# Kernel tuning notes

Hardware: AMD Instinct MI355X
Metric: run time of the kernel (lower is better)

## Reference

```python
import jax, jax.numpy as jnp
import numpy as np


def setup_inputs() -> dict:
    key = jax.random.key(0)
    k1, k2 = jax.random.split(key)
    B, T, D, K = 16, 800, 256, 64
    x = jax.random.normal(k1, (B, T, D), dtype=jnp.float32)
    mu = jax.random.normal(k2, (K, D), dtype=jnp.float32)
    prec = jnp.ones((K,), dtype=jnp.float32)
    return {"x": x, "mu": mu, "prec": prec}


def reference(x, mu, prec):
    # x: (B,T,D), mu: (K,D), prec: (K,)
    delta = x[:, :, None, :] - mu[None, None, :, :]          # (B,T,K,D)
    dist = jnp.sum(delta * delta, axis=-1)                   # (B,T,K) dist_pow=2
    llk = -(prec * prec) * dist                              # use_bias=False -> bias=0
    r = jax.nn.softmax(llk, axis=-1)                         # softmax over components K
    r = r / (jnp.sum(r, axis=1, keepdims=True) + 1e-9)       # normalize over time T
    pool = jnp.einsum('btk,btkd->bkd', r, delta)             # weighted sum over T
    return pool.reshape(x.shape[0], -1)                      # (B, K*D)
```

## Files before the change

### kernel.cpp

```cpp
#include <hip/hip_runtime.h>

#define B_ 16
#define T_ 800
#define D_ 256
#define K_ 64
#define NTILE 13

typedef __attribute__((ext_vector_type(8))) short short8v;
typedef __attribute__((ext_vector_type(4))) float f32x4v;

__device__ __forceinline__ ushort bf16rn(float v) {
    unsigned int b = __float_as_uint(v);
    return (ushort)((b + 0x7fffu + ((b >> 16) & 1u)) >> 16);
}
__device__ __forceinline__ float bf16hi(ushort h) {
    return __uint_as_float(((unsigned int)h) << 16);
}

__global__ __launch_bounds__(256) void prep(
    const float* __restrict__ x, const float* __restrict__ mu, const float* __restrict__ prec,
    float* __restrict__ xx_g, float* __restrict__ mm_g, float* __restrict__ p2_g)
{
    const int bid = blockIdx.x, tid = threadIdx.x;
    if (bid < 3200) {
        const int row = bid * 4 + (tid >> 6), lane = tid & 63;
        float4 v = ((const float4*)x)[(size_t)row * 64 + lane];
        float s = v.x*v.x + v.y*v.y + v.z*v.z + v.w*v.w;
        #pragma unroll
        for (int off = 32; off > 0; off >>= 1) s += __shfl_xor(s, off);
        if (lane == 0) xx_g[row] = s;
    } else if (bid < 3216) {
        const int row = (bid - 3200) * 4 + (tid >> 6), lane = tid & 63;
        float4 v = ((const float4*)mu)[(size_t)row * 64 + lane];
        float s = v.x*v.x + v.y*v.y + v.z*v.z + v.w*v.w;
        #pragma unroll
        for (int off = 32; off > 0; off >>= 1) s += __shfl_xor(s, off);
        if (lane == 0) mm_g[row] = s;
    } else {
        if (tid < 64) { float p = prec[tid]; p2_g[tid] = p * p; }
    }
}

__global__ __launch_bounds__(256, 1) void kernelAB(
    const float* __restrict__ x, const float* __restrict__ mu,
    const float* __restrict__ xx_g, const float* __restrict__ mm_g,
    const float* __restrict__ p2_g,
    float* __restrict__ Pp, float* __restrict__ Spart)
{
    __shared__ ushort xh_s[64 * 264];
    __shared__ ushort xl_s[64 * 264];
    __shared__ ushort muh_s[64 * 264];
    __shared__ ushort mul_s[64 * 264];
    __shared__ ushort rtT_s[64 * 72];
    __shared__ float xxs[64], mms[64], p2s[64];
    __shared__ float sred[4][64];

    const int tid  = threadIdx.x;
    const int lane = tid & 63;
    const int w    = tid >> 6;
    const int m    = lane & 15;
    const int q    = lane >> 4;
    const int b    = blockIdx.x / NTILE;
    const int tile = blockIdx.x % NTILE;
    const int t0   = tile * 64;

    if (tid < 64)       xxs[tid]       = xx_g[b * T_ + min(t0 + tid, T_ - 1)];
    else if (tid < 128) mms[tid - 64]  = mm_g[tid - 64];
    else if (tid < 192) p2s[tid - 128] = p2_g[tid - 128];

    #pragma unroll 4
    for (int jj = 0; jj < 16; ++jj) {
        const int idx = tid + jj * 256;
        const int row = idx >> 6, c = idx & 63;
        int trow = t0 + row; if (trow > T_ - 1) trow = T_ - 1;
        float4 v = ((const float4*)x)[(size_t)(b * T_ + trow) * 64 + c];
        ushort4 h, l;
        h.x = bf16rn(v.x); l.x = bf16rn(v.x - bf16hi(h.x));
        h.y = bf16rn(v.y); l.y = bf16rn(v.y - bf16hi(h.y));
        h.z = bf16rn(v.z); l.z = bf16rn(v.z - bf16hi(h.z));
        h.w = bf16rn(v.w); l.w = bf16rn(v.w - bf16hi(h.w));
        *(ushort4*)&xh_s[row * 264 + c * 4] = h;
        *(ushort4*)&xl_s[row * 264 + c * 4] = l;
    }
    #pragma unroll 4
    for (int jj = 0; jj < 16; ++jj) {
        const int idx = tid + jj * 256;
        const int row = idx >> 6, c = idx & 63;
        float4 v = ((const float4*)mu)[(size_t)row * 64 + c];
        ushort4 h, l;
        h.x = bf16rn(v.x); l.x = bf16rn(v.x - bf16hi(h.x));
        h.y = bf16rn(v.y); l.y = bf16rn(v.y - bf16hi(h.y));
        h.z = bf16rn(v.z); l.z = bf16rn(v.z - bf16hi(h.z));
        h.w = bf16rn(v.w); l.w = bf16rn(v.w - bf16hi(h.w));
        *(ushort4*)&muh_s[row * 264 + c * 4] = h;
        *(ushort4*)&mul_s[row * 264 + c * 4] = l;
    }
    __syncthreads();

    f32x4v acc[4];
    #pragma unroll
    for (int nt = 0; nt < 4; ++nt) acc[nt] = (f32x4v){0.f, 0.f, 0.f, 0.f};

    #pragma unroll 2
    for (int c = 0; c < 8; ++c) {
        const int ao = (w * 16 + m) * 264 + c * 32 + q * 8;
        short8v ah = *(const short8v*)&xh_s[ao];
        short8v al = *(const short8v*)&xl_s[ao];
        #pragma unroll
        for (int nt = 0; nt < 4; ++nt) {
            const int bo = (nt * 16 + m) * 264 + c * 32 + q * 8;
            short8v bh = *(const short8v*)&muh_s[bo];
            short8v bl = *(const short8v*)&mul_s[bo];
            acc[nt] = __builtin_amdgcn_mfma_f32_16x16x32_bf16(ah, bh, acc[nt], 0, 0, 0);
            acc[nt] = __builtin_amdgcn_mfma_f32_16x16x32_bf16(ah, bl, acc[nt], 0, 0, 0);
            acc[nt] = __builtin_amdgcn_mfma_f32_16x16x32_bf16(al, bh, acc[nt], 0, 0, 0);
        }
    }

    float mmk[4], p2k[4];
    #pragma unroll
    for (int nt = 0; nt < 4; ++nt) { mmk[nt] = mms[nt * 16 + m]; p2k[nt] = p2s[nt * 16 + m]; }

    ushort4 rp[4];
    float sacc[4] = {0.f, 0.f, 0.f, 0.f};
    #pragma unroll
    for (int r = 0; r < 4; ++r) {
        const int tl = w * 16 + q * 4 + r;
        const float xxv = xxs[tl];
        const bool valid = (t0 + tl) < T_;
        float llk[4];
        #pragma unroll
        for (int nt = 0; nt < 4; ++nt)
            llk[nt] = p2k[nt] * (2.f * acc[nt][r] - xxv - mmk[nt]);
        float mx = fmaxf(fmaxf(llk[0], llk[1]), fmaxf(llk[2], llk[3]));
        mx = fmaxf(mx, __shfl_xor(mx, 1)); mx = fmaxf(mx, __shfl_xor(mx, 2));
        mx = fmaxf(mx, __shfl_xor(mx, 4)); mx = fmaxf(mx, __shfl_xor(mx, 8));
        float e[4], ps = 0.f;
        #pragma unroll
        for (int nt = 0; nt < 4; ++nt) { e[nt] = __expf(llk[nt] - mx); ps += e[nt]; }
        ps += __shfl_xor(ps, 1); ps += __shfl_xor(ps, 2);
        ps += __shfl_xor(ps, 4); ps += __shfl_xor(ps, 8);
        const float inv = valid ? (1.f / ps) : 0.f;
        #pragma unroll
        for (int nt = 0; nt < 4; ++nt) {
            float rv = e[nt] * inv;
            sacc[nt] += rv;
            ((ushort*)&rp[nt])[r] = bf16rn(rv);
        }
    }
    #pragma unroll
    for (int nt = 0; nt < 4; ++nt)
        *(ushort4*)&rtT_s[(nt * 16 + m) * 72 + w * 16 + q * 4] = rp[nt];
    #pragma unroll
    for (int nt = 0; nt < 4; ++nt) {
        sacc[nt] += __shfl_xor(sacc[nt], 16);
        sacc[nt] += __shfl_xor(sacc[nt], 32);
    }
    if (q == 0) {
        #pragma unroll
        for (int nt = 0; nt < 4; ++nt) sred[w][nt * 16 + m] = sacc[nt];
    }
    __syncthreads();

    if (tid < 64) {
        float s = sred[0][tid] + sred[1][tid] + sred[2][tid] + sred[3][tid];
        Spart[((size_t)b * NTILE + tile) * K_ + tid] = s;
    }

    {
        const int tp = tid & 31, dg = tid >> 5;
        #pragma unroll
        for (int c = 0; c < 4; ++c) {
            short8v a0 = *(const short8v*)&xh_s[(2 * tp)     * 264 + dg * 32 + c * 8];
            short8v a1 = *(const short8v*)&xh_s[(2 * tp + 1) * 264 + dg * 32 + c * 8];
            short8v b0 = *(const short8v*)&xl_s[(2 * tp)     * 264 + dg * 32 + c * 8];
            short8v b1 = *(const short8v*)&xl_s[(2 * tp + 1) * 264 + dg * 32 + c * 8];
            #pragma unroll
            for (int j = 0; j < 8; ++j) {
                const int d = dg * 32 + c * 8 + j;
                const int widx = (tp & 3) + 4 * ((tp >> 2) ^ (d & 7));
                ushort2 hv, lv;
                hv.x = (ushort)a0[j]; hv.y = (ushort)a1[j];
                lv.x = (ushort)b0[j]; lv.y = (ushort)b1[j];
                *(ushort2*)&muh_s[d * 64 + widx * 2] = hv;
                *(ushort2*)&mul_s[d * 64 + widx * 2] = lv;
            }
        }
    }
    __syncthreads();

    f32x4v acc2[16];
    #pragma unroll
    for (int nt = 0; nt < 16; ++nt) acc2[nt] = (f32x4v){0.f, 0.f, 0.f, 0.f};

    #pragma unroll
    for (int tc = 0; tc < 2; ++tc) {
        short8v ar = *(const short8v*)&rtT_s[(w * 16 + m) * 72 + tc * 32 + q * 8];
        #pragma unroll
        for (int nt = 0; nt < 16; ++nt) {
            const int drow = nt * 16 + m;
            const int eoff = ((tc * 4 + q) ^ (drow & 7)) * 8;
            short8v bh = *(const short8v*)&muh_s[drow * 64 + eoff];
            short8v bl = *(const short8v*)&mul_s[drow * 64 + eoff];
            acc2[nt] = __builtin_amdgcn_mfma_f32_16x16x32_bf16(ar, bh, acc2[nt], 0, 0, 0);
            acc2[nt] = __builtin_amdgcn_mfma_f32_16x16x32_bf16(ar, bl, acc2[nt], 0, 0, 0);
        }
    }

    float* Pb = Pp + ((size_t)(b * NTILE + tile)) * K_ * D_;
    #pragma unroll
    for (int nt = 0; nt < 16; ++nt) {
        #pragma unroll
        for (int r = 0; r < 4; ++r)
            Pb[(size_t)(w * 16 + q * 4 + r) * D_ + nt * 16 + m] = acc2[nt][r];
    }
}

__global__ __launch_bounds__(256) void kernelC(
    const float* __restrict__ Pp, const float* __restrict__ Spart,
    const float* __restrict__ mu, float* __restrict__ out)
{
    const int o4 = blockIdx.x * 256 + threadIdx.x;
    const int d4 = o4 & 63;
    const int k  = (o4 >> 6) & 63;
    const int b  = o4 >> 12;

    float s = 0.f;
    #pragma unroll
    for (int p = 0; p < NTILE; ++p)
        s += Spart[((size_t)b * NTILE + p) * K_ + k];

    float4 acc = make_float4(0.f, 0.f, 0.f, 0.f);
    #pragma unroll
    for (int p = 0; p < NTILE; ++p) {
        float4 v = ((const float4*)Pp)[((size_t)(b * NTILE + p) * K_ + k) * (D_ / 4) + d4];
        acc.x += v.x; acc.y += v.y; acc.z += v.z; acc.w += v.w;
    }
    const float inv = 1.f / (s + 1e-9f);
    const float sm  = s * inv;
    const float4 m = ((const float4*)mu)[k * 64 + d4];
    float4 o;
    o.x = acc.x * inv - sm * m.x;
    o.y = acc.y * inv - sm * m.y;
    o.z = acc.z * inv - sm * m.z;
    o.w = acc.w * inv - sm * m.w;
    ((float4*)out)[o4] = o;
}

extern "C" void kernel_launch(void* const* d_in, const int* in_sizes, int n_in,
                              void* d_out, int out_size, void* d_ws, size_t ws_size,
                              hipStream_t stream) {
    const float* x    = (const float*)d_in[0];
    const float* mu   = (const float*)d_in[1];
    const float* prec = (const float*)d_in[2];
    float* out = (float*)d_out;

    float* Pp    = (float*)d_ws;
    float* Spart = Pp + (size_t)B_ * NTILE * K_ * D_;
    float* xx_g  = Spart + (size_t)B_ * NTILE * K_;
    float* mm_g  = xx_g + (size_t)B_ * T_;
    float* p2_g  = mm_g + 64;

    prep<<<3217, 256, 0, stream>>>(x, mu, prec, xx_g, mm_g, p2_g);
    kernelAB<<<B_ * NTILE, 256, 0, stream>>>(x, mu, xx_g, mm_g, p2_g, Pp, Spart);
    kernelC<<<256, 256, 0, stream>>>(Pp, Spart, mu, out);
}
```

Before: 80.27 us.

## Fuse norm prep into main kernel and double block to 512 threads

Removes the separate prep kernel by computing row squared norms of x and mu during the shared-memory staging loads, and computes prec squared in-kernel. The main kernel now runs 512 threads per block: each of the 8 waves handles half the components in the distance GEMM and half the D columns in the pooling GEMM. The softmax max and sum are combined across the two wave halves through shared memory with extra barriers. This saves a kernel launch and a pass over x and aims for more latency hiding per block, at the cost of added synchronisation.

Result: no change. 80.42 us (+0.2%).

```diff
diff --git a/kernel.cpp b/kernel.cpp
--- a/kernel.cpp
+++ b/kernel.cpp
@@ -17,34 +17,9 @@
     return __uint_as_float(((unsigned int)h) << 16);
 }
 
-__global__ __launch_bounds__(256) void prep(
-    const float* __restrict__ x, const float* __restrict__ mu, const float* __restrict__ prec,
-    float* __restrict__ xx_g, float* __restrict__ mm_g, float* __restrict__ p2_g)
-{
-    const int bid = blockIdx.x, tid = threadIdx.x;
-    if (bid < 3200) {
-        const int row = bid * 4 + (tid >> 6), lane = tid & 63;
-        float4 v = ((const float4*)x)[(size_t)row * 64 + lane];
-        float s = v.x*v.x + v.y*v.y + v.z*v.z + v.w*v.w;
-        #pragma unroll
-        for (int off = 32; off > 0; off >>= 1) s += __shfl_xor(s, off);
-        if (lane == 0) xx_g[row] = s;
-    } else if (bid < 3216) {
-        const int row = (bid - 3200) * 4 + (tid >> 6), lane = tid & 63;
-        float4 v = ((const float4*)mu)[(size_t)row * 64 + lane];
-        float s = v.x*v.x + v.y*v.y + v.z*v.z + v.w*v.w;
-        #pragma unroll
-        for (int off = 32; off > 0; off >>= 1) s += __shfl_xor(s, off);
-        if (lane == 0) mm_g[row] = s;
-    } else {
-        if (tid < 64) { float p = prec[tid]; p2_g[tid] = p * p; }
-    }
-}
-
-__global__ __launch_bounds__(256, 1) void kernelAB(
+__global__ __launch_bounds__(512, 1) void kernelAB(
     const float* __restrict__ x, const float* __restrict__ mu,
-    const float* __restrict__ xx_g, const float* __restrict__ mm_g,
-    const float* __restrict__ p2_g,
+    const float* __restrict__ prec,
     float* __restrict__ Pp, float* __restrict__ Spart)
 {
     __shared__ ushort xh_s[64 * 264];
@@ -53,6 +28,7 @@
     __shared__ ushort mul_s[64 * 264];
     __shared__ ushort rtT_s[64 * 72];
     __shared__ float xxs[64], mms[64], p2s[64];
+    __shared__ float red_m[64][2], red_s[64][2];
     __shared__ float sred[4][64];
 
     const int tid  = threadIdx.x;
@@ -64,101 +40,132 @@
     const int tile = blockIdx.x % NTILE;
     const int t0   = tile * 64;
 
-    if (tid < 64)       xxs[tid]       = xx_g[b * T_ + min(t0 + tid, T_ - 1)];
-    else if (tid < 128) mms[tid - 64]  = mm_g[tid - 64];
-    else if (tid < 192) p2s[tid - 128] = p2_g[tid - 128];
+    if (tid < 64) { float p = prec[tid]; p2s[tid] = p * p; }
 
     #pragma unroll 4
-    for (int jj = 0; jj < 16; ++jj) {
-        const int idx = tid + jj * 256;
-        const int row = idx >> 6, c = idx & 63;
+    for (int jj = 0; jj < 8; ++jj) {
+        const int idx = tid + jj * 512;
+        const int row = idx >> 6;
+        const int cc  = idx & 63;
         int trow = t0 + row; if (trow > T_ - 1) trow = T_ - 1;
-        float4 v = ((const float4*)x)[(size_t)(b * T_ + trow) * 64 + c];
+        float4 v = ((const float4*)x)[(size_t)(b * T_ + trow) * 64 + cc];
+        float sq = v.x*v.x + v.y*v.y + v.z*v.z + v.w*v.w;
+        #pragma unroll
+        for (int off = 32; off > 0; off >>= 1) sq += __shfl_xor(sq, off);
+        if (lane == 0) xxs[row] = sq;
         ushort4 h, l;
         h.x = bf16rn(v.x); l.x = bf16rn(v.x - bf16hi(h.x));
         h.y = bf16rn(v.y); l.y = bf16rn(v.y - bf16hi(h.y));
         h.z = bf16rn(v.z); l.z = bf16rn(v.z - bf16hi(h.z));
         h.w = bf16rn(v.w); l.w = bf16rn(v.w - bf16hi(h.w));
-        *(ushort4*)&xh_s[row * 264 + c * 4] = h;
-        *(ushort4*)&xl_s[row * 264 + c * 4] = l;
+        *(ushort4*)&xh_s[row * 264 + cc * 4] = h;
+        *(ushort4*)&xl_s[row * 264 + cc * 4] = l;
     }
     #pragma unroll 4
-    for (int jj = 0; jj < 16; ++jj) {
-        const int idx = tid + jj * 256;
-        const int row = idx >> 6, c = idx & 63;
-        float4 v = ((const float4*)mu)[(size_t)row * 64 + c];
+    for (int jj = 0; jj < 8; ++jj) {
+        const int idx = tid + jj * 512;
+        const int row = idx >> 6, cc = idx & 63;
+        float4 v = ((const float4*)mu)[(size_t)row * 64 + cc];
+        float sq = v.x*v.x + v.y*v.y + v.z*v.z + v.w*v.w;
+        #pragma unroll
+        for (int off = 32; off > 0; off >>= 1) sq += __shfl_xor(sq, off);
+        if (lane == 0) mms[row] = sq;
         ushort4 h, l;
         h.x = bf16rn(v.x); l.x = bf16rn(v.x - bf16hi(h.x));
         h.y = bf16rn(v.y); l.y = bf16rn(v.y - bf16hi(h.y));
         h.z = bf16rn(v.z); l.z = bf16rn(v.z - bf16hi(h.z));
         h.w = bf16rn(v.w); l.w = bf16rn(v.w - bf16hi(h.w));
-        *(ushort4*)&muh_s[row * 264 + c * 4] = h;
-        *(ushort4*)&mul_s[row * 264 + c * 4] = l;
-    }
-    __syncthreads();
-
-    f32x4v acc[4];
-    #pragma unroll
-    for (int nt = 0; nt < 4; ++nt) acc[nt] = (f32x4v){0.f, 0.f, 0.f, 0.f};
+        *(ushort4*)&muh_s[row * 264 + cc * 4] = h;
+        *(ushort4*)&mul_s[row * 264 + cc * 4] = l;
+    }
+    __syncthreads();
+
+    const int tg = w & 3, kh = w >> 2;
+    f32x4v acc[2];
+    #pragma unroll
+    for (int ntl = 0; ntl < 2; ++ntl) acc[ntl] = (f32x4v){0.f, 0.f, 0.f, 0.f};
 
     #pragma unroll 2
     for (int c = 0; c < 8; ++c) {
-        const int ao = (w * 16 + m) * 264 + c * 32 + q * 8;
+        const int ao = (tg * 16 + m) * 264 + c * 32 + q * 8;
         short8v ah = *(const short8v*)&xh_s[ao];
         short8v al = *(const short8v*)&xl_s[ao];
         #pragma unroll
-        for (int nt = 0; nt < 4; ++nt) {
-            const int bo = (nt * 16 + m) * 264 + c * 32 + q * 8;
+        for (int ntl = 0; ntl < 2; ++ntl) {
+            const int bo = ((kh * 2 + ntl) * 16 + m) * 264 + c * 32 + q * 8;
             short8v bh = *(const short8v*)&muh_s[bo];
             short8v bl = *(const short8v*)&mul_s[bo];
-            acc[nt] = __builtin_amdgcn_mfma_f32_16x16x32_bf16(ah, bh, acc[nt], 0, 0, 0);
-            acc[nt] = __builtin_amdgcn_mfma_f32_16x16x32_bf16(ah, bl, acc[nt], 0, 0, 0);
-            acc[nt] = __builtin_amdgcn_mfma_f32_16x16x32_bf16(al, bh, acc[nt], 0, 0, 0);
-        }
-    }
-
-    float mmk[4], p2k[4];
-    #pragma unroll
-    for (int nt = 0; nt < 4; ++nt) { mmk[nt] = mms[nt * 16 + m]; p2k[nt] = p2s[nt * 16 + m]; }
-
-    ushort4 rp[4];
-    float sacc[4] = {0.f, 0.f, 0.f, 0.f};
-    #pragma unroll
-    for (int r = 0; r < 4; ++r) {
-        const int tl = w * 16 + q * 4 + r;
+            acc[ntl] = __builtin_amdgcn_mfma_f32_16x16x32_bf16(ah, bh, acc[ntl], 0, 0, 0);
+            acc[ntl] = __builtin_amdgcn_mfma_f32_16x16x32_bf16(ah, bl, acc[ntl], 0, 0, 0);
+            acc[ntl] = __builtin_amdgcn_mfma_f32_16x16x32_bf16(al, bh, acc[ntl], 0, 0, 0);
+        }
+    }
+
+    float p2k[2], mmk[2];
+    #pragma unroll
+    for (int ntl = 0; ntl < 2; ++ntl) {
+        const int kk = (kh * 2 + ntl) * 16 + m;
+        p2k[ntl] = p2s[kk]; mmk[ntl] = mms[kk];
+    }
+
+    float llk[2][4];
+    #pragma unroll
+    for (int r = 0; r < 4; ++r) {
+        const int tl = tg * 16 + q * 4 + r;
         const float xxv = xxs[tl];
-        const bool valid = (t0 + tl) < T_;
-        float llk[4];
-        #pragma unroll
-        for (int nt = 0; nt < 4; ++nt)
-            llk[nt] = p2k[nt] * (2.f * acc[nt][r] - xxv - mmk[nt]);
-        float mx = fmaxf(fmaxf(llk[0], llk[1]), fmaxf(llk[2], llk[3]));
-        mx = fmaxf(mx, __shfl_xor(mx, 1)); mx = fmaxf(mx, __shfl_xor(mx, 2));
-        mx = fmaxf(mx, __shfl_xor(mx, 4)); mx = fmaxf(mx, __shfl_xor(mx, 8));
-        float e[4], ps = 0.f;
-        #pragma unroll
-        for (int nt = 0; nt < 4; ++nt) { e[nt] = __expf(llk[nt] - mx); ps += e[nt]; }
+        #pragma unroll
+        for (int ntl = 0; ntl < 2; ++ntl)
+            llk[ntl][r] = p2k[ntl] * (2.f * acc[ntl][r] - xxv - mmk[ntl]);
+    }
+    #pragma unroll
+    for (int r = 0; r < 4; ++r) {
+        float pm = fmaxf(llk[0][r], llk[1][r]);
+        pm = fmaxf(pm, __shfl_xor(pm, 1)); pm = fmaxf(pm, __shfl_xor(pm, 2));
+        pm = fmaxf(pm, __shfl_xor(pm, 4)); pm = fmaxf(pm, __shfl_xor(pm, 8));
+        if (m == 0) red_m[tg * 16 + q * 4 + r][kh] = pm;
+    }
+    __syncthreads();
+    float e[2][4], psum[4];
+    #pragma unroll
+    for (int r = 0; r < 4; ++r) {
+        const int tl = tg * 16 + q * 4 + r;
+        const float gm = fmaxf(red_m[tl][0], red_m[tl][1]);
+        float ps = 0.f;
+        #pragma unroll
+        for (int ntl = 0; ntl < 2; ++ntl) { e[ntl][r] = __expf(llk[ntl][r] - gm); ps += e[ntl][r]; }
         ps += __shfl_xor(ps, 1); ps += __shfl_xor(ps, 2);
         ps += __shfl_xor(ps, 4); ps += __shfl_xor(ps, 8);
-        const float inv = valid ? (1.f / ps) : 0.f;
-        #pragma unroll
-        for (int nt = 0; nt < 4; ++nt) {
-            float rv = e[nt] * inv;
-            sacc[nt] += rv;
-            ((ushort*)&rp[nt])[r] = bf16rn(rv);
-        }
-    }
-    #pragma unroll
-    for (int nt = 0; nt < 4; ++nt)
-        *(ushort4*)&rtT_s[(nt * 16 + m) * 72 + w * 16 + q * 4] = rp[nt];
-    #pragma unroll
-    for (int nt = 0; nt < 4; ++nt) {
-        sacc[nt] += __shfl_xor(sacc[nt], 16);
-        sacc[nt] += __shfl_xor(sacc[nt], 32);
+        psum[r] = ps;
+        if (m == 0) red_s[tl][kh] = ps;
+    }
+    __syncthreads();
+    float sacc[2] = {0.f, 0.f};
+    ushort4 rp[2];
+    #pragma unroll
+    for (int r = 0; r < 4; ++r) {
+        const int tl = tg * 16 + q * 4 + r;
+        const float gs = red_s[tl][0] + red_s[tl][1];
+        const bool valid = (t0 + tl) < T_;
+        const float inv = valid ? (1.f / gs) : 0.f;
+        #pragma unroll
+        for (int ntl = 0; ntl < 2; ++ntl) {
+            float rv = e[ntl][r] * inv;
+            sacc[ntl] += rv;
+            ((ushort*)&rp[ntl])[r] = bf16rn(rv);
+        }
+    }
+    #pragma unroll
+    for (int ntl = 0; ntl < 2; ++ntl)
+        *(ushort4*)&rtT_s[((kh * 2 + ntl) * 16 + m) * 72 + tg * 16 + q * 4] = rp[ntl];
+    #pragma unroll
+    for (int ntl = 0; ntl < 2; ++ntl) {
+        sacc[ntl] += __shfl_xor(sacc[ntl], 16);
+        sacc[ntl] += __shfl_xor(sacc[ntl], 32);
     }
     if (q == 0) {
         #pragma unroll
-        for (int nt = 0; nt < 4; ++nt) sred[w][nt * 16 + m] = sacc[nt];
+        for (int ntl = 0; ntl < 2; ++ntl)
+            sred[tg][(kh * 2 + ntl) * 16 + m] = sacc[ntl];
     }
     __syncthreads();
 
@@ -170,14 +177,14 @@
     {
         const int tp = tid & 31, dg = tid >> 5;
         #pragma unroll
-        for (int c = 0; c < 4; ++c) {
-            short8v a0 = *(const short8v*)&xh_s[(2 * tp)     * 264 + dg * 32 + c * 8];
-            short8v a1 = *(const short8v*)&xh_s[(2 * tp + 1) * 264 + dg * 32 + c * 8];
-            short8v b0 = *(const short8v*)&xl_s[(2 * tp)     * 264 + dg * 32 + c * 8];
-            short8v b1 = *(const short8v*)&xl_s[(2 * tp + 1) * 264 + dg * 32 + c * 8];
+        for (int c = 0; c < 2; ++c) {
+            short8v a0 = *(const short8v*)&xh_s[(2 * tp)     * 264 + dg * 16 + c * 8];
+            short8v a1 = *(const short8v*)&xh_s[(2 * tp + 1) * 264 + dg * 16 + c * 8];
+            short8v b0 = *(const short8v*)&xl_s[(2 * tp)     * 264 + dg * 16 + c * 8];
+            short8v b1 = *(const short8v*)&xl_s[(2 * tp + 1) * 264 + dg * 16 + c * 8];
             #pragma unroll
             for (int j = 0; j < 8; ++j) {
-                const int d = dg * 32 + c * 8 + j;
+                const int d = dg * 16 + c * 8 + j;
                 const int widx = (tp & 3) + 4 * ((tp >> 2) ^ (d & 7));
                 ushort2 hv, lv;
                 hv.x = (ushort)a0[j]; hv.y = (ushort)a1[j];
@@ -189,30 +196,31 @@
     }
     __syncthreads();
 
-    f32x4v acc2[16];
-    #pragma unroll
-    for (int nt = 0; nt < 16; ++nt) acc2[nt] = (f32x4v){0.f, 0.f, 0.f, 0.f};
+    const int kg = w & 3, dh = w >> 2;
+    f32x4v acc2[8];
+    #pragma unroll
+    for (int ntl = 0; ntl < 8; ++ntl) acc2[ntl] = (f32x4v){0.f, 0.f, 0.f, 0.f};
 
     #pragma unroll
     for (int tc = 0; tc < 2; ++tc) {
-        short8v ar = *(const short8v*)&rtT_s[(w * 16 + m) * 72 + tc * 32 + q * 8];
-        #pragma unroll
-        for (int nt = 0; nt < 16; ++nt) {
-            const int drow = nt * 16 + m;
+        short8v ar = *(const short8v*)&rtT_s[(kg * 16 + m) * 72 + tc * 32 + q * 8];
+        #pragma unroll
+        for (int ntl = 0; ntl < 8; ++ntl) {
+            const int drow = (dh * 8 + ntl) * 16 + m;
             const int eoff = ((tc * 4 + q) ^ (drow & 7)) * 8;
             short8v bh = *(const short8v*)&muh_s[drow * 64 + eoff];
             short8v bl = *(const short8v*)&mul_s[drow * 64 + eoff];
-            acc2[nt] = __builtin_amdgcn_mfma_f32_16x16x32_bf16(ar, bh, acc2[nt], 0, 0, 0);
-            acc2[nt] = __builtin_amdgcn_mfma_f32_16x16x32_bf16(ar, bl, acc2[nt], 0, 0, 0);
+            acc2[ntl] = __builtin_amdgcn_mfma_f32_16x16x32_bf16(ar, bh, acc2[ntl], 0, 0, 0);
+            acc2[ntl] = __builtin_amdgcn_mfma_f32_16x16x32_bf16(ar, bl, acc2[ntl], 0, 0, 0);
         }
     }
 
     float* Pb = Pp + ((size_t)(b * NTILE + tile)) * K_ * D_;
     #pragma unroll
-    for (int nt = 0; nt < 16; ++nt) {
+    for (int ntl = 0; ntl < 8; ++ntl) {
         #pragma unroll
         for (int r = 0; r < 4; ++r)
-            Pb[(size_t)(w * 16 + q * 4 + r) * D_ + nt * 16 + m] = acc2[nt][r];
+            Pb[(size_t)(kg * 16 + q * 4 + r) * D_ + (dh * 8 + ntl) * 16 + m] = acc2[ntl][r];
     }
 }
 
@@ -257,11 +265,7 @@
 
     float* Pp    = (float*)d_ws;
     float* Spart = Pp + (size_t)B_ * NTILE * K_ * D_;
-    float* xx_g  = Spart + (size_t)B_ * NTILE * K_;
-    float* mm_g  = xx_g + (size_t)B_ * T_;
-    float* p2_g  = mm_g + 64;
-
-    prep<<<3217, 256, 0, stream>>>(x, mu, prec, xx_g, mm_g, p2_g);
-    kernelAB<<<B_ * NTILE, 256, 0, stream>>>(x, mu, xx_g, mm_g, p2_g, Pp, Spart);
+
+    kernelAB<<<B_ * NTILE, 512, 0, stream>>>(x, mu, prec, Pp, Spart);
     kernelC<<<256, 256, 0, stream>>>(Pp, Spart, mu, out);
 }
```
